# Performance work log

Hardware: AMD Instinct MI355X
Metric: run time of the kernel (lower is better)

Reference implementation:

```python
import jax, jax.numpy as jnp
import numpy as np

N_NODES = 80000
N_EDGES = 1280000
IN_CH = 128
OUT_CH = 32
HID = 2 * OUT_CH


def gcn_conv(x, W, b, src, dst, n_nodes):
    """PyG GCNConv with self-loops and symmetric normalization.
    out[i] = b + sum_{j->i} deg(j)^-1/2 deg(i)^-1/2 (x_j @ W)
    """
    loop = jnp.arange(n_nodes, dtype=src.dtype)
    s = jnp.concatenate([src, loop])  # [E+N]
    d = jnp.concatenate([dst, loop])  # [E+N]
    deg = jax.ops.segment_sum(jnp.ones_like(d, dtype=x.dtype), d,
                              num_segments=n_nodes)  # in-degree incl. self loop
    dinv = jnp.where(deg > 0, jax.lax.rsqrt(deg), 0.0)
    norm = dinv[s] * dinv[d]  # [E+N]
    h = x @ W  # [N, F_out] dense transform first (fewer flops when F_out < F_in)
    msg = h[s] * norm[:, None]  # [E+N, F_out] gather + scale
    out = jax.ops.segment_sum(msg, d, num_segments=n_nodes)  # scatter-add
    return out + b


def setup_inputs() -> dict:
    key = jax.random.key(0)
    k1, k2, k3, k4 = jax.random.split(key, 4)
    x = jax.random.normal(k1, (N_NODES, IN_CH), dtype=jnp.float32)
    edge_index = jax.random.randint(k2, (2, N_EDGES), 0, N_NODES, dtype=jnp.int64)
    W1 = jax.random.normal(k3, (IN_CH, HID), dtype=jnp.float32) / np.sqrt(IN_CH)
    b1 = jnp.zeros((HID,), dtype=jnp.float32)
    W2 = jax.random.normal(k4, (HID, OUT_CH), dtype=jnp.float32) / np.sqrt(HID)
    b2 = jnp.zeros((OUT_CH,), dtype=jnp.float32)
    return {"x": x, "edge_index": edge_index, "W1": W1, "b1": b1,
            "W2": W2, "b2": b2}


def reference(x, edge_index, W1, b1, W2, b2):
    src, dst = edge_index[0], edge_index[1]
    h = jax.nn.relu(gcn_conv(x, W1, b1, src, dst, N_NODES))
    return gcn_conv(h, W2, b2, src, dst, N_NODES)
```

## Files before the change

kernel.cpp:

```cpp
#include <hip/hip_runtime.h>
#include <hip/hip_fp16.h>

#define N_NODES 80000
#define N_EDGES 1280000
#define IN_CH 128
#define HID 64
#define OUT_CH 32

#define NBUCK 625
#define CAP 3072
#define BIN_BLOCKS 256

typedef float vf2 __attribute__((ext_vector_type(2)));
typedef float vf4 __attribute__((ext_vector_type(4)));
typedef short short8 __attribute__((ext_vector_type(8)));
typedef float floatx4 __attribute__((ext_vector_type(4)));

__device__ __forceinline__ unsigned bf16rn(float x) {
    unsigned u = __float_as_uint(x);
    return (u + 0x7FFFu + ((u >> 16) & 1u)) >> 16;
}
__device__ __forceinline__ unsigned packbf2(float a, float b) {
    return bf16rn(a) | (bf16rn(b) << 16);
}
__device__ __forceinline__ float hl(unsigned u) {
    return __half2float(__ushort_as_half((unsigned short)(u & 0xFFFFu)));
}
__device__ __forceinline__ float hh(unsigned u) {
    return __half2float(__ushort_as_half((unsigned short)(u >> 16)));
}
__device__ __forceinline__ unsigned pack2h(float a, float b) {
    return (unsigned)__half_as_ushort(__float2half_rn(a)) |
           ((unsigned)__half_as_ushort(__float2half_rn(b)) << 16);
}

__global__ __launch_bounds__(256) void k_bin_gemm1(
        const int* __restrict__ src, const int* __restrict__ dst,
        int* __restrict__ gcur, unsigned int* __restrict__ binned,
        const float* __restrict__ x, const float* __restrict__ W1,
        unsigned short* __restrict__ h1h) {
    __shared__ unsigned short smem_u[26112];
    int bid = blockIdx.x, t = threadIdx.x;
    if (bid < BIN_BLOCKS) {
        int* hist = (int*)smem_u;
        int* lcur = hist + NBUCK;
        const int chunk = N_EDGES / BIN_BLOCKS;
        int e0 = bid * chunk;
        int e1 = e0 + chunk;
        for (int i = t; i < NBUCK; i += 256) hist[i] = 0;
        __syncthreads();
        for (int e = e0 + t; e < e1; e += 256)
            atomicAdd(&hist[dst[e] >> 7], 1);
        __syncthreads();
        for (int i = t; i < NBUCK; i += 256) {
            int h = hist[i];
            lcur[i] = h ? atomicAdd(&gcur[i], h) : 0;
        }
        __syncthreads();
        for (int e = e0 + t; e < e1; e += 256) {
            int d = dst[e];
            int bk = d >> 7;
            int pos = atomicAdd(&lcur[bk], 1);
            if (pos < CAP)
                binned[(size_t)bk * CAP + pos] =
                    (unsigned int)src[e] | ((unsigned int)(d & 127) << 17);
        }
    } else {
        unsigned short* sX = smem_u;
        unsigned short* sWT = smem_u + 128 * 136;
        long long nb = (long long)(bid - BIN_BLOCKS) * 128;
        for (int it = 0; it < 16; ++it) {
            int idx = t + it * 256;
            int node = idx >> 5, k4 = (idx & 31) * 4;
            float4 v = *(const float4*)&x[(nb + node) * IN_CH + k4];
            unsigned u0 = packbf2(v.x, v.y), u1 = packbf2(v.z, v.w);
            *(uint2*)&sX[node * 136 + k4] = (uint2){u0, u1};
        }
        for (int it = 0; it < 8; ++it) {
            int idx = t + it * 256;
            int k = idx >> 4, c4 = (idx & 15) * 4;
            float4 w = *(const float4*)&W1[k * 64 + c4];
            sWT[(c4 + 0) * 136 + k] = (unsigned short)bf16rn(w.x);
            sWT[(c4 + 1) * 136 + k] = (unsigned short)bf16rn(w.y);
            sWT[(c4 + 2) * 136 + k] = (unsigned short)bf16rn(w.z);
            sWT[(c4 + 3) * 136 + k] = (unsigned short)bf16rn(w.w);
        }
        __syncthreads();
        int wv = t >> 6, lane = t & 63;
        int lm = lane & 15, q = lane >> 4;
        int m0 = wv * 32;
        floatx4 acc[2][4];
#pragma unroll
        for (int i = 0; i < 2; ++i)
#pragma unroll
            for (int j = 0; j < 4; ++j) acc[i][j] = (floatx4){0.f, 0.f, 0.f, 0.f};
#pragma unroll
        for (int kk = 0; kk < 128; kk += 32) {
            short8 a0 = *(short8*)&sX[(m0 + lm) * 136 + kk + q * 8];
            short8 a1 = *(short8*)&sX[(m0 + 16 + lm) * 136 + kk + q * 8];
#pragma unroll
            for (int ct = 0; ct < 4; ++ct) {
                short8 bfr = *(short8*)&sWT[(ct * 16 + lm) * 136 + kk + q * 8];
                acc[0][ct] = __builtin_amdgcn_mfma_f32_16x16x32_bf16(a0, bfr, acc[0][ct], 0, 0, 0);
                acc[1][ct] = __builtin_amdgcn_mfma_f32_16x16x32_bf16(a1, bfr, acc[1][ct], 0, 0, 0);
            }
        }
#pragma unroll
        for (int mt = 0; mt < 2; ++mt)
#pragma unroll
            for (int ct = 0; ct < 4; ++ct)
#pragma unroll
                for (int r = 0; r < 4; ++r) {
                    long long node = nb + m0 + mt * 16 + q * 4 + r;
                    int c = ct * 16 + lm;
                    h1h[node * 64 + c] = __half_as_ushort(__float2half_rn(acc[mt][ct][r]));
                }
    }
}

__global__ __launch_bounds__(256) void k_csr(const unsigned int* __restrict__ binned,
                                             const int* __restrict__ cnt,
                                             int* __restrict__ csr,
                                             int* __restrict__ rs, int* __restrict__ re,
                                             float* __restrict__ dinv) {
    __shared__ int deg[128];
    __shared__ int scan[128];
    __shared__ int cur[128];
    int bk = blockIdx.x, t = threadIdx.x;
    int n_e = min(cnt[bk], CAP);
    const unsigned int* eb = binned + (size_t)bk * CAP;
    if (t < 128) deg[t] = 0;
    __syncthreads();
    for (int i = t; i < n_e; i += 256) atomicAdd(&deg[eb[i] >> 17], 1);
    __syncthreads();
    if (t < 128) scan[t] = deg[t];
    __syncthreads();
    for (int off = 1; off < 128; off <<= 1) {
        int v = (t < 128 && t >= off) ? scan[t - off] : 0;
        __syncthreads();
        if (t < 128) scan[t] += v;
        __syncthreads();
    }
    if (t < 128) {
        int incl = scan[t];
        int s = incl - deg[t];
        cur[t] = s;
        int n = bk * 128 + t;
        int base = bk * CAP;
        rs[n] = base + s;
        re[n] = base + incl;
        dinv[n] = rsqrtf((float)(deg[t] + 1));
    }
    __syncthreads();
    for (int i = t; i < n_e; i += 256) {
        unsigned int p = eb[i];
        int dL = p >> 17;
        int pos = atomicAdd(&cur[dL], 1);
        csr[bk * CAP + pos] = (int)(p & 0x1FFFF);
    }
}

__global__ __launch_bounds__(256) void k_agg64(
        const unsigned int* __restrict__ h1u, const int* __restrict__ csr,
        const int* __restrict__ rs_, const int* __restrict__ re_,
        const float* __restrict__ dinv, const float* __restrict__ b1,
        float* __restrict__ h2) {
    int n = blockIdx.x * 4 + (threadIdx.x >> 6);
    int lane = threadIdx.x & 63;
    int half = lane >> 5, fo = lane & 31;
    int a = rs_[n], b = re_[n];
    float ax = 0.f, ay = 0.f;
    int e = a + half;
    for (; e + 6 < b; e += 8) {
        int s0 = csr[e], s1 = csr[e + 2], s2 = csr[e + 4], s3 = csr[e + 6];
        unsigned u0 = h1u[(size_t)s0 * 32 + fo]; float d0 = dinv[s0];
        unsigned u1 = h1u[(size_t)s1 * 32 + fo]; float d1 = dinv[s1];
        unsigned u2 = h1u[(size_t)s2 * 32 + fo]; float d2 = dinv[s2];
        unsigned u3 = h1u[(size_t)s3 * 32 + fo]; float d3 = dinv[s3];
        ax += d0 * hl(u0); ay += d0 * hh(u0);
        ax += d1 * hl(u1); ay += d1 * hh(u1);
        ax += d2 * hl(u2); ay += d2 * hh(u2);
        ax += d3 * hl(u3); ay += d3 * hh(u3);
    }
    for (; e < b; e += 2) {
        int s = csr[e];
        unsigned u = h1u[(size_t)s * 32 + fo];
        float d = dinv[s];
        ax += d * hl(u); ay += d * hh(u);
    }
    ax += __shfl_down(ax, 32);
    ay += __shfl_down(ay, 32);
    if (half == 0) {
        float dn = dinv[n];
        unsigned un = h1u[(size_t)n * 32 + fo];
        ax += dn * hl(un); ay += dn * hh(un);
        float2 bb = *(const float2*)&b1[2 * fo];
        float2 o = {fmaxf(dn * ax + bb.x, 0.f), fmaxf(dn * ay + bb.y, 0.f)};
        *(float2*)&h2[(size_t)n * 64 + 2 * fo] = o;
    }
}

__global__ __launch_bounds__(256) void k_gemm2(const float* __restrict__ h2,
                                               const float* __restrict__ W2,
                                               unsigned int* __restrict__ g2u) {
    __shared__ float sX[64 * 68];
    __shared__ float sW[64 * 32];
    int t = threadIdx.x;
    long long nb = (long long)blockIdx.x * 64;
    for (int i = t * 4; i < 64 * 32; i += 1024) {
        *(float4*)&sW[i] = *(const float4*)&W2[i];
    }
    for (int r = 0; r < 4; ++r) {
        int n = (t >> 4) + r * 16;
        int k4 = (t & 15) * 4;
        *(float4*)&sX[n * 68 + k4] = *(const float4*)&h2[(nb + n) * HID + k4];
    }
    __syncthreads();
    int tx = t & 7, ty = t >> 3;
    float acc0[4] = {0, 0, 0, 0}, acc1[4] = {0, 0, 0, 0};
#pragma unroll 4
    for (int k = 0; k < 64; ++k) {
        float4 w = *(float4*)&sW[k * 32 + tx * 4];
        float x0 = sX[(ty * 2 + 0) * 68 + k];
        float x1 = sX[(ty * 2 + 1) * 68 + k];
        acc0[0] += x0 * w.x; acc0[1] += x0 * w.y; acc0[2] += x0 * w.z; acc0[3] += x0 * w.w;
        acc1[0] += x1 * w.x; acc1[1] += x1 * w.y; acc1[2] += x1 * w.z; acc1[3] += x1 * w.w;
    }
    long long n = nb + ty * 2;
    uint2 p0 = {pack2h(acc0[0], acc0[1]), pack2h(acc0[2], acc0[3])};
    *(uint2*)&g2u[n * 16 + tx * 2] = p0;
    uint2 p1 = {pack2h(acc1[0], acc1[1]), pack2h(acc1[2], acc1[3])};
    *(uint2*)&g2u[(n + 1) * 16 + tx * 2] = p1;
}

__global__ __launch_bounds__(256) void k_agg32(
        const unsigned int* __restrict__ g2u, const int* __restrict__ csr,
        const int* __restrict__ rs_, const int* __restrict__ re_,
        const float* __restrict__ dinv, const float* __restrict__ b2,
        float* __restrict__ outp) {
    int n = blockIdx.x * 4 + (threadIdx.x >> 6);
    int lane = threadIdx.x & 63;
    int oc = lane >> 3, fo = lane & 7;
    int a = rs_[n], b = re_[n];
    float ax = 0.f, ay = 0.f, az = 0.f, aw = 0.f;
    int e = a + oc;
    for (; e + 8 < b; e += 16) {
        int s0 = csr[e], s1 = csr[e + 8];
        uint2 u0 = *(const uint2*)&g2u[(size_t)s0 * 16 + 2 * fo]; float d0 = dinv[s0];
        uint2 u1 = *(const uint2*)&g2u[(size_t)s1 * 16 + 2 * fo]; float d1 = dinv[s1];
        ax += d0 * hl(u0.x); ay += d0 * hh(u0.x);
        az += d0 * hl(u0.y); aw += d0 * hh(u0.y);
        ax += d1 * hl(u1.x); ay += d1 * hh(u1.x);
        az += d1 * hl(u1.y); aw += d1 * hh(u1.y);
    }
    for (; e < b; e += 8) {
        int s = csr[e];
        uint2 u = *(const uint2*)&g2u[(size_t)s * 16 + 2 * fo];
        float d = dinv[s];
        ax += d * hl(u.x); ay += d * hh(u.x);
        az += d * hl(u.y); aw += d * hh(u.y);
    }
    ax += __shfl_down(ax, 32); ay += __shfl_down(ay, 32);
    az += __shfl_down(az, 32); aw += __shfl_down(aw, 32);
    ax += __shfl_down(ax, 16); ay += __shfl_down(ay, 16);
    az += __shfl_down(az, 16); aw += __shfl_down(aw, 16);
    ax += __shfl_down(ax, 8);  ay += __shfl_down(ay, 8);
    az += __shfl_down(az, 8);  aw += __shfl_down(aw, 8);
    if (oc == 0) {
        float dn = dinv[n];
        uint2 un = *(const uint2*)&g2u[(size_t)n * 16 + 2 * fo];
        ax += dn * hl(un.x); ay += dn * hh(un.x);
        az += dn * hl(un.y); aw += dn * hh(un.y);
        float4 bb = *(const float4*)&b2[4 * fo];
        vf4 o = {dn * ax + bb.x, dn * ay + bb.y, dn * az + bb.z, dn * aw + bb.w};
        __builtin_nontemporal_store(o, (vf4*)&outp[(size_t)n * 32 + 4 * fo]);
    }
}

static inline size_t align256(size_t x) { return (x + 255) & ~(size_t)255; }

extern "C" void kernel_launch(void* const* d_in, const int* in_sizes, int n_in,
                              void* d_out, int out_size, void* d_ws, size_t ws_size,
                              hipStream_t stream) {
    const float* x  = (const float*)d_in[0];
    const int*   ei = (const int*)d_in[1];
    const float* W1 = (const float*)d_in[2];
    const float* b1 = (const float*)d_in[3];
    const float* W2 = (const float*)d_in[4];
    const float* b2 = (const float*)d_in[5];
    float* out = (float*)d_out;

    const int* src = ei;
    const int* dst = ei + N_EDGES;

    char* ws = (char*)d_ws;
    size_t off = 0;
    int* gcur = (int*)(ws + off);              off = align256(off + NBUCK * 4);
    unsigned int* binned = (unsigned int*)(ws + off);
                                               off = align256(off + (size_t)NBUCK * CAP * 4);
    int* csr = (int*)(ws + off);               off = align256(off + (size_t)NBUCK * CAP * 4);
    int* rs  = (int*)(ws + off);               off = align256(off + (size_t)N_NODES * 4);
    int* re  = (int*)(ws + off);               off = align256(off + (size_t)N_NODES * 4);
    float* dinv = (float*)(ws + off);          off = align256(off + (size_t)N_NODES * 4);
    unsigned short* h1h = (unsigned short*)(ws + off);
                                               off = align256(off + (size_t)N_NODES * 64 * 2);
    float* h2 = (float*)(ws + off);            off = align256(off + (size_t)N_NODES * HID * 4);
    unsigned int* g2u = (unsigned int*)h1h;

    (void)hipMemsetAsync(gcur, 0, NBUCK * 4, stream);
    k_bin_gemm1<<<BIN_BLOCKS + N_NODES / 128, 256, 0, stream>>>(src, dst, gcur, binned,
                                                                x, W1, h1h);
    k_csr<<<NBUCK, 256, 0, stream>>>(binned, gcur, csr, rs, re, dinv);
    k_agg64<<<N_NODES / 4, 256, 0, stream>>>((const unsigned int*)h1h, csr, rs, re,
                                             dinv, b1, h2);
    k_gemm2<<<N_NODES / 64, 256, 0, stream>>>(h2, W2, g2u);
    k_agg32<<<N_NODES / 4, 256, 0, stream>>>(g2u, csr, rs, re, dinv, b2, out);
}
```

Baseline: 215.7 us.

## Fuse layer-1 aggregation with second GEMM, two nodes per wavefront

Merges the 64-wide aggregation kernel with the dense h2@W2 transform. Each block now keeps W2 and b1 in shared memory, and each wavefront handles two nodes with 16 lanes per edge stream and uint2 loads. The ReLU output goes to shared memory and is immediately multiplied by W2, then written as packed half g2. This removes one kernel launch and the fp32 h2 round trip through global memory. The cost is per-block W2 staging, extra block-wide syncs, and a scalar 64-step shared-memory dot product per lane.

```diff
diff --git a/kernel.cpp b/kernel.cpp
--- a/kernel.cpp
+++ b/kernel.cpp
@@ -164,73 +164,68 @@
         const unsigned int* __restrict__ h1u, const int* __restrict__ csr,
         const int* __restrict__ rs_, const int* __restrict__ re_,
         const float* __restrict__ dinv, const float* __restrict__ b1,
-        float* __restrict__ h2) {
-    int n = blockIdx.x * 4 + (threadIdx.x >> 6);
-    int lane = threadIdx.x & 63;
-    int half = lane >> 5, fo = lane & 31;
+        const float* __restrict__ W2, unsigned int* __restrict__ g2u) {
+    __shared__ float sW2[64 * 32];
+    __shared__ float sB1[64];
+    __shared__ float sH2[4][2][64];
+    int t = threadIdx.x;
+    for (int i = t * 2; i < 64 * 32; i += 512)
+        *(vf2*)&sW2[i] = *(const vf2*)&W2[i];
+    if (t < 32) *(vf2*)&sB1[t * 2] = *(const vf2*)&b1[t * 2];
+
+    int wv = t >> 6, lane = t & 63;
+    int nd = lane >> 5;
+    int q  = (lane >> 4) & 1;
+    int fo = lane & 15;
+    long long n = (long long)blockIdx.x * 8 + wv * 2 + nd;
     int a = rs_[n], b = re_[n];
-    float ax = 0.f, ay = 0.f;
-    int e = a + half;
+    float ax = 0.f, ay = 0.f, az = 0.f, aw = 0.f;
+    int e = a + q;
     for (; e + 6 < b; e += 8) {
         int s0 = csr[e], s1 = csr[e + 2], s2 = csr[e + 4], s3 = csr[e + 6];
-        unsigned u0 = h1u[(size_t)s0 * 32 + fo]; float d0 = dinv[s0];
-        unsigned u1 = h1u[(size_t)s1 * 32 + fo]; float d1 = dinv[s1];
-        unsigned u2 = h1u[(size_t)s2 * 32 + fo]; float d2 = dinv[s2];
-        unsigned u3 = h1u[(size_t)s3 * 32 + fo]; float d3 = dinv[s3];
-        ax += d0 * hl(u0); ay += d0 * hh(u0);
-        ax += d1 * hl(u1); ay += d1 * hh(u1);
-        ax += d2 * hl(u2); ay += d2 * hh(u2);
-        ax += d3 * hl(u3); ay += d3 * hh(u3);
+        uint2 u0 = *(const uint2*)&h1u[(size_t)s0 * 32 + 2 * fo]; float d0 = dinv[s0];
+        uint2 u1 = *(const uint2*)&h1u[(size_t)s1 * 32 + 2 * fo]; float d1 = dinv[s1];
+        uint2 u2 = *(const uint2*)&h1u[(size_t)s2 * 32 + 2 * fo]; float d2 = dinv[s2];
+        uint2 u3 = *(const uint2*)&h1u[(size_t)s3 * 32 + 2 * fo]; float d3 = dinv[s3];
+        ax += d0 * hl(u0.x); ay += d0 * hh(u0.x); az += d0 * hl(u0.y); aw += d0 * hh(u0.y);
+        ax += d1 * hl(u1.x); ay += d1 * hh(u1.x); az += d1 * hl(u1.y); aw += d1 * hh(u1.y);
+        ax += d2 * hl(u2.x); ay += d2 * hh(u2.x); az += d2 * hl(u2.y); aw += d2 * hh(u2.y);
+        ax += d3 * hl(u3.x); ay += d3 * hh(u3.x); az += d3 * hl(u3.y); aw += d3 * hh(u3.y);
     }
     for (; e < b; e += 2) {
         int s = csr[e];
-        unsigned u = h1u[(size_t)s * 32 + fo];
+        uint2 u = *(const uint2*)&h1u[(size_t)s * 32 + 2 * fo];
         float d = dinv[s];
-        ax += d * hl(u); ay += d * hh(u);
-    }
-    ax += __shfl_down(ax, 32);
-    ay += __shfl_down(ay, 32);
-    if (half == 0) {
+        ax += d * hl(u.x); ay += d * hh(u.x); az += d * hl(u.y); aw += d * hh(u.y);
+    }
+    ax += __shfl_down(ax, 16); ay += __shfl_down(ay, 16);
+    az += __shfl_down(az, 16); aw += __shfl_down(aw, 16);
+    __syncthreads();
+    if (q == 0) {
         float dn = dinv[n];
-        unsigned un = h1u[(size_t)n * 32 + fo];
-        ax += dn * hl(un); ay += dn * hh(un);
-        float2 bb = *(const float2*)&b1[2 * fo];
-        float2 o = {fmaxf(dn * ax + bb.x, 0.f), fmaxf(dn * ay + bb.y, 0.f)};
-        *(float2*)&h2[(size_t)n * 64 + 2 * fo] = o;
-    }
-}
-
-__global__ __launch_bounds__(256) void k_gemm2(const float* __restrict__ h2,
-                                               const float* __restrict__ W2,
-                                               unsigned int* __restrict__ g2u) {
-    __shared__ float sX[64 * 68];
-    __shared__ float sW[64 * 32];
-    int t = threadIdx.x;
-    long long nb = (long long)blockIdx.x * 64;
-    for (int i = t * 4; i < 64 * 32; i += 1024) {
-        *(float4*)&sW[i] = *(const float4*)&W2[i];
-    }
-    for (int r = 0; r < 4; ++r) {
-        int n = (t >> 4) + r * 16;
-        int k4 = (t & 15) * 4;
-        *(float4*)&sX[n * 68 + k4] = *(const float4*)&h2[(nb + n) * HID + k4];
-    }
-    __syncthreads();
-    int tx = t & 7, ty = t >> 3;
-    float acc0[4] = {0, 0, 0, 0}, acc1[4] = {0, 0, 0, 0};
-#pragma unroll 4
-    for (int k = 0; k < 64; ++k) {
-        float4 w = *(float4*)&sW[k * 32 + tx * 4];
-        float x0 = sX[(ty * 2 + 0) * 68 + k];
-        float x1 = sX[(ty * 2 + 1) * 68 + k];
-        acc0[0] += x0 * w.x; acc0[1] += x0 * w.y; acc0[2] += x0 * w.z; acc0[3] += x0 * w.w;
-        acc1[0] += x1 * w.x; acc1[1] += x1 * w.y; acc1[2] += x1 * w.z; acc1[3] += x1 * w.w;
-    }
-    long long n = nb + ty * 2;
-    uint2 p0 = {pack2h(acc0[0], acc0[1]), pack2h(acc0[2], acc0[3])};
-    *(uint2*)&g2u[n * 16 + tx * 2] = p0;
-    uint2 p1 = {pack2h(acc1[0], acc1[1]), pack2h(acc1[2], acc1[3])};
-    *(uint2*)&g2u[(n + 1) * 16 + tx * 2] = p1;
+        uint2 un = *(const uint2*)&h1u[(size_t)n * 32 + 2 * fo];
+        ax += dn * hl(un.x); ay += dn * hh(un.x);
+        az += dn * hl(un.y); aw += dn * hh(un.y);
+        float4 bb = *(const float4*)&sB1[4 * fo];
+        vf4 h2v = {fmaxf(dn * ax + bb.x, 0.f), fmaxf(dn * ay + bb.y, 0.f),
+                   fmaxf(dn * az + bb.z, 0.f), fmaxf(dn * aw + bb.w, 0.f)};
+        *(vf4*)&sH2[wv][nd][4 * fo] = h2v;
+    }
+    __syncthreads();
+    int col = lane & 31;
+    int nd2 = lane >> 5;
+    const float* hrow = sH2[wv][nd2];
+    float g = 0.f;
+#pragma unroll
+    for (int k = 0; k < 64; ++k) g += hrow[k] * sW2[k * 32 + col];
+    float g1 = __shfl_down(g, 1);
+    float g2v = __shfl_down(g, 2);
+    float g3 = __shfl_down(g, 3);
+    if ((lane & 3) == 0) {
+        long long nn = (long long)blockIdx.x * 8 + wv * 2 + nd2;
+        uint2 p = {pack2h(g, g1), pack2h(g2v, g3)};
+        *(uint2*)&g2u[(size_t)nn * 16 + (col >> 1)] = p;
+    }
 }
 
 __global__ __launch_bounds__(256) void k_agg32(
@@ -304,15 +299,14 @@
     float* dinv = (float*)(ws + off);          off = align256(off + (size_t)N_NODES * 4);
     unsigned short* h1h = (unsigned short*)(ws + off);
                                                off = align256(off + (size_t)N_NODES * 64 * 2);
-    float* h2 = (float*)(ws + off);            off = align256(off + (size_t)N_NODES * HID * 4);
-    unsigned int* g2u = (unsigned int*)h1h;
+    unsigned int* g2u = (unsigned int*)(ws + off);
+                                               off = align256(off + (size_t)N_NODES * 16 * 4);
 
     (void)hipMemsetAsync(gcur, 0, NBUCK * 4, stream);
     k_bin_gemm1<<<BIN_BLOCKS + N_NODES / 128, 256, 0, stream>>>(src, dst, gcur, binned,
                                                                 x, W1, h1h);
     k_csr<<<NBUCK, 256, 0, stream>>>(binned, gcur, csr, rs, re, dinv);
-    k_agg64<<<N_NODES / 4, 256, 0, stream>>>((const unsigned int*)h1h, csr, rs, re,
-                                             dinv, b1, h2);
-    k_gemm2<<<N_NODES / 64, 256, 0, stream>>>(h2, W2, g2u);
+    k_agg64<<<N_NODES / 8, 256, 0, stream>>>((const unsigned int*)h1h, csr, rs, re,
+                                             dinv, b1, W2, g2u);
     k_agg32<<<N_NODES / 4, 256, 0, stream>>>(g2u, csr, rs, re, dinv, b2, out);
 }
```

Result: faster. 204.9 us (-5.0%).
